# Performance work log

Hardware: AMD Instinct MI355X
Metric: run time of the kernel (lower is better)

## Reference

```python
import jax, jax.numpy as jnp
import numpy as np

NEG_FILL = -100.0  # matches torch new_full(-100.0) init for scatter-amax


def reference(x, part_labels, parts_num=16):
    # x: (n, c, s, h, w) float; part_labels: (n, s, h, w) int in [0, parts_num)
    n, c, s, h, w = x.shape
    hw = h * w
    ns = n * s
    # (n s) c (h w)
    feat = jnp.transpose(x, (0, 2, 1, 3, 4)).reshape(ns, c, hw)
    labels = part_labels.reshape(ns, hw).astype(jnp.int32)

    b3 = jnp.arange(ns)[:, None, None]          # (ns,1,1)
    ch = jnp.arange(c)[None, :, None]            # (1,c,1)
    lbl3 = labels[:, None, :]                    # (ns,1,hw) -> broadcasts to (ns,c,hw)

    pooled_sum = jnp.zeros((ns, c, parts_num), x.dtype).at[b3, ch, lbl3].add(feat)
    b2 = jnp.arange(ns)[:, None]
    pooled_count = jnp.zeros((ns, parts_num), x.dtype).at[b2, labels].add(1.0)  # (ns,P)
    pooled_max = jnp.full((ns, c, parts_num), NEG_FILL, x.dtype).at[b3, ch, lbl3].max(feat)

    count = pooled_count[:, None, :]             # (ns,1,P)
    pooled_mean = pooled_sum / jnp.maximum(count, 1.0)
    pooled_max = jnp.where(count > 0, pooled_max, 0.0)
    pooled = pooled_mean + pooled_max            # (ns,c,P)
    # (n s) c p -> n c s p
    return jnp.transpose(pooled.reshape(n, s, c, parts_num), (0, 2, 1, 3))


def setup_inputs() -> dict:
    key = jax.random.key(0)
    k1, k2 = jax.random.split(key)
    n, c, s, h, w = 16, 256, 32, 16, 11
    parts_num = 16
    x = jax.random.normal(k1, (n, c, s, h, w), dtype=jnp.float32)
    part_labels = jax.random.randint(k2, (n, s, h, w), 0, parts_num, dtype=jnp.int64)
    return {"x": x, "part_labels": part_labels, "parts_num": parts_num}
```

## Files before the change

kernel.cpp:

```cpp
#include <hip/hip_runtime.h>


constexpr int C   = 256;
constexpr int S   = 32;
constexpr int HW  = 176;
constexpr int P   = 16;
constexpr int ROW = S * HW;
constexpr int GC  = 8;
constexpr int NS2 = 2;
constexpr int PITCH = 180;
constexpr float NEG_FILL = -100.0f;

__device__ __forceinline__ void barrier_lgkm() {
    asm volatile("s_waitcnt lgkmcnt(0)\n\ts_barrier" ::: "memory");
}

__global__ __launch_bounds__(256) void hpp_kernel(
    const float* __restrict__ x,
    const int*   __restrict__ labels,
    float*       __restrict__ out)
{
    __shared__ float tile[GC * NS2 * PITCH];
    __shared__ __align__(4) unsigned char posmap[NS2][HW];
    __shared__ int cnt[NS2 * P];
    __shared__ int base[NS2 * P];

    const int tid = threadIdx.x;
    const int blk = blockIdx.x;
    const int nsp = blk >> 5, cg = blk & 31;
    const int n   = nsp >> 4, sp = nsp & 15;
    const int s   = sp * 2;

    const int* ln = labels + (size_t)(n * S + s) * HW;
    int lab0 = 0, lab1 = 0;
    if (tid < HW) { lab0 = ln[tid]; lab1 = ln[HW + tid]; }

    const float* xb = x + (size_t)(n * C + cg * GC) * ROW + s * HW;
    const int f0 = tid, f1 = tid + 256, f2 = tid + 512;
    const int r0 = f0 / 88, j0 = f0 - r0 * 88;
    const int r1 = f1 / 88, j1 = f1 - r1 * 88;
    const int r2 = f2 / 88, j2 = f2 - r2 * 88;
    float4 v0 = *(const float4*)(xb + (size_t)r0 * ROW + j0 * 4);
    float4 v1 = *(const float4*)(xb + (size_t)r1 * ROW + j1 * 4);
    float4 v2 = make_float4(0.f, 0.f, 0.f, 0.f);
    const bool has2 = (f2 < GC * 88);
    if (has2) v2 = *(const float4*)(xb + (size_t)r2 * ROW + j2 * 4);

    if (tid < NS2 * P) cnt[tid] = 0;
    barrier_lgkm();
    int a0 = 0, a1 = 0;
    if (tid < HW) {
        a0 = atomicAdd(&cnt[lab0], 1);
        a1 = atomicAdd(&cnt[P + lab1], 1);
    }
    barrier_lgkm();
    if (tid < NS2 * P) {
        int acc = 0;
        const int b0 = tid & ~(P - 1);
        for (int q = b0; q < tid; ++q) acc += cnt[q];
        base[tid] = acc;
    }
    barrier_lgkm();
    if (tid < HW) {
        posmap[0][tid] = (unsigned char)(base[lab0] + a0);
        posmap[1][tid] = (unsigned char)(base[P + lab1] + a1);
    }
    barrier_lgkm();

    {
        const int q0 = j0 * 4, s20 = (q0 >= HW), h0 = q0 - s20 * HW;
        unsigned pm0 = *(const unsigned*)&posmap[s20][h0];
        float* t0 = &tile[(r0 * 2 + s20) * PITCH];
        t0[pm0 & 0xFF] = v0.x; t0[(pm0 >> 8) & 0xFF] = v0.y;
        t0[(pm0 >> 16) & 0xFF] = v0.z; t0[pm0 >> 24] = v0.w;

        const int q1 = j1 * 4, s21 = (q1 >= HW), h1 = q1 - s21 * HW;
        unsigned pm1 = *(const unsigned*)&posmap[s21][h1];
        float* t1 = &tile[(r1 * 2 + s21) * PITCH];
        t1[pm1 & 0xFF] = v1.x; t1[(pm1 >> 8) & 0xFF] = v1.y;
        t1[(pm1 >> 16) & 0xFF] = v1.z; t1[pm1 >> 24] = v1.w;

        if (has2) {
            const int q2 = j2 * 4, s22 = (q2 >= HW), h2 = q2 - s22 * HW;
            unsigned pm2 = *(const unsigned*)&posmap[s22][h2];
            float* t2 = &tile[(r2 * 2 + s22) * PITCH];
            t2[pm2 & 0xFF] = v2.x; t2[(pm2 >> 8) & 0xFF] = v2.y;
            t2[(pm2 >> 16) & 0xFF] = v2.z; t2[pm2 >> 24] = v2.w;
        }
    }
    barrier_lgkm();

    const int p   = tid >> 4;
    const int low = tid & 15;
    const int sp2 = low & 1;
    const int c   = low >> 1;
    const int idx = sp2 * P + p;
    const int k   = cnt[idx];
    int off       = base[idx];
    const float* tc = &tile[low * PITCH];

    float s0 = 0.f, s1 = 0.f, m0 = NEG_FILL, m1 = NEG_FILL;
    int rem = k;
    int h = (4 - (off & 3)) & 3; if (h > rem) h = rem;
    if (h > 0) { float a = tc[off];     s0 += a; m0 = fmaxf(m0, a); }
    if (h > 1) { float a = tc[off + 1]; s1 += a; m1 = fmaxf(m1, a); }
    if (h > 2) { float a = tc[off + 2]; s0 += a; m0 = fmaxf(m0, a); }
    off += h; rem -= h;
    int n4 = rem >> 2;
    for (int i = 0; i < n4; ++i) {
        float4 q = *(const float4*)&tc[off];
        s0 += q.x; m0 = fmaxf(m0, q.x);
        s1 += q.y; m1 = fmaxf(m1, q.y);
        s0 += q.z; m0 = fmaxf(m0, q.z);
        s1 += q.w; m1 = fmaxf(m1, q.w);
        off += 4;
    }
    rem &= 3;
    if (rem > 0) { float a = tc[off];     s0 += a; m0 = fmaxf(m0, a); }
    if (rem > 1) { float a = tc[off + 1]; s1 += a; m1 = fmaxf(m1, a); }
    if (rem > 2) { float a = tc[off + 2]; s0 += a; m0 = fmaxf(m0, a); }

    float res = (k > 0) ? (s0 + s1) / (float)k + fmaxf(m0, m1) : 0.f;
    out[((size_t)(n * C + cg * GC + c) * S + (s + sp2)) * P + p] = res;
}

extern "C" void kernel_launch(void* const* d_in, const int* in_sizes, int n_in,
                              void* d_out, int out_size, void* d_ws, size_t ws_size,
                              hipStream_t stream) {
    const float* x      = (const float*)d_in[0];
    const int*   labels = (const int*)d_in[1];
    float*       out    = (float*)d_out;

    const int ns_total = in_sizes[1] / HW;
    const int nblk     = (ns_total / NS2) * (C / GC);
    hpp_kernel<<<nblk, 256, 0, stream>>>(x, labels, out);
}
```

Baseline: 136.3 us.

## Shrink blocks to one 64-thread wavefront, replacing barriers with LDS waitcnt fences

Each block now handles 2 channels instead of 8 using a single 64-lane wavefront, so the s_barrier instructions can be dropped and only lgkmcnt waits remain. Labels are loaded as int4 vectors and each lane histograms four labels, and the gather/reduce mapping is rebuilt for the smaller tile. This removes block-level synchronisation and raises the block count, but each block now recomputes the label histogram and posmap for 2 channels instead of 8, so that per-block work is repeated four times more often.

```diff
diff --git a/kernel.cpp b/kernel.cpp
--- a/kernel.cpp
+++ b/kernel.cpp
@@ -6,16 +6,16 @@
 constexpr int HW  = 176;
 constexpr int P   = 16;
 constexpr int ROW = S * HW;
-constexpr int GC  = 8;
+constexpr int GC  = 2;
 constexpr int NS2 = 2;
 constexpr int PITCH = 180;
 constexpr float NEG_FILL = -100.0f;
 
-__device__ __forceinline__ void barrier_lgkm() {
-    asm volatile("s_waitcnt lgkmcnt(0)\n\ts_barrier" ::: "memory");
+__device__ __forceinline__ void fence_lds() {
+    asm volatile("s_waitcnt lgkmcnt(0)" ::: "memory");
 }
 
-__global__ __launch_bounds__(256) void hpp_kernel(
+__global__ __launch_bounds__(64) void hpp_kernel(
     const float* __restrict__ x,
     const int*   __restrict__ labels,
     float*       __restrict__ out)
@@ -27,77 +27,105 @@
 
     const int tid = threadIdx.x;
     const int blk = blockIdx.x;
-    const int nsp = blk >> 5, cg = blk & 31;
+    const int cg2 = blk & 127;
+    const int nsp = blk >> 7;
     const int n   = nsp >> 4, sp = nsp & 15;
     const int s   = sp * 2;
+    const int c0  = cg2 * 2;
 
     const int* ln = labels + (size_t)(n * S + s) * HW;
-    int lab0 = 0, lab1 = 0;
-    if (tid < HW) { lab0 = ln[tid]; lab1 = ln[HW + tid]; }
+    int4 L0 = ((const int4*)ln)[tid];
+    int4 L1 = make_int4(0, 0, 0, 0);
+    const bool hasL1 = (tid < 24);
+    if (hasL1) L1 = ((const int4*)ln)[tid + 64];
 
-    const float* xb = x + (size_t)(n * C + cg * GC) * ROW + s * HW;
-    const int f0 = tid, f1 = tid + 256, f2 = tid + 512;
-    const int r0 = f0 / 88, j0 = f0 - r0 * 88;
-    const int r1 = f1 / 88, j1 = f1 - r1 * 88;
-    const int r2 = f2 / 88, j2 = f2 - r2 * 88;
-    float4 v0 = *(const float4*)(xb + (size_t)r0 * ROW + j0 * 4);
+    const float* xb = x + (size_t)(n * C + c0) * ROW + s * HW;
+    const int j0 = tid;
+    const int r1 = (tid < 24) ? 0 : 1;
+    const int j1 = (tid < 24) ? tid + 64 : tid - 24;
+    const int j2 = tid + 40;
+    const bool has2 = (tid < 48);
+    float4 v0 = *(const float4*)(xb + (size_t)0 * ROW + j0 * 4);
     float4 v1 = *(const float4*)(xb + (size_t)r1 * ROW + j1 * 4);
     float4 v2 = make_float4(0.f, 0.f, 0.f, 0.f);
-    const bool has2 = (f2 < GC * 88);
-    if (has2) v2 = *(const float4*)(xb + (size_t)r2 * ROW + j2 * 4);
+    if (has2) v2 = *(const float4*)(xb + (size_t)1 * ROW + j2 * 4);
 
     if (tid < NS2 * P) cnt[tid] = 0;
-    barrier_lgkm();
-    int a0 = 0, a1 = 0;
-    if (tid < HW) {
-        a0 = atomicAdd(&cnt[lab0], 1);
-        a1 = atomicAdd(&cnt[P + lab1], 1);
+    fence_lds();
+    const int row0 = (tid >= 44);
+    int a0, a1, a2, a3;
+    {
+        int* c = &cnt[row0 * P];
+        a0 = atomicAdd(&c[L0.x], 1);
+        a1 = atomicAdd(&c[L0.y], 1);
+        a2 = atomicAdd(&c[L0.z], 1);
+        a3 = atomicAdd(&c[L0.w], 1);
     }
-    barrier_lgkm();
+    int b0 = 0, b1 = 0, b2 = 0, b3 = 0;
+    if (hasL1) {
+        int* c = &cnt[P];
+        b0 = atomicAdd(&c[L1.x], 1);
+        b1 = atomicAdd(&c[L1.y], 1);
+        b2 = atomicAdd(&c[L1.z], 1);
+        b3 = atomicAdd(&c[L1.w], 1);
+    }
+    fence_lds();
     if (tid < NS2 * P) {
         int acc = 0;
-        const int b0 = tid & ~(P - 1);
-        for (int q = b0; q < tid; ++q) acc += cnt[q];
+        const int g0 = tid & ~(P - 1);
+        for (int q = g0; q < tid; ++q) acc += cnt[q];
         base[tid] = acc;
     }
-    barrier_lgkm();
-    if (tid < HW) {
-        posmap[0][tid] = (unsigned char)(base[lab0] + a0);
-        posmap[1][tid] = (unsigned char)(base[P + lab1] + a1);
+    fence_lds();
+    {
+        const int hw0 = (tid * 4) - row0 * 176;
+        const int* bs = &base[row0 * P];
+        posmap[row0][hw0    ] = (unsigned char)(bs[L0.x] + a0);
+        posmap[row0][hw0 + 1] = (unsigned char)(bs[L0.y] + a1);
+        posmap[row0][hw0 + 2] = (unsigned char)(bs[L0.z] + a2);
+        posmap[row0][hw0 + 3] = (unsigned char)(bs[L0.w] + a3);
+        if (hasL1) {
+            const int hw1 = 80 + tid * 4;
+            const int* b1s = &base[P];
+            posmap[1][hw1    ] = (unsigned char)(b1s[L1.x] + b0);
+            posmap[1][hw1 + 1] = (unsigned char)(b1s[L1.y] + b1);
+            posmap[1][hw1 + 2] = (unsigned char)(b1s[L1.z] + b2);
+            posmap[1][hw1 + 3] = (unsigned char)(b1s[L1.w] + b3);
+        }
     }
-    barrier_lgkm();
+    fence_lds();
 
     {
-        const int q0 = j0 * 4, s20 = (q0 >= HW), h0 = q0 - s20 * HW;
+        const int s20 = (j0 >= 44), h0 = j0 * 4 - s20 * 176;
         unsigned pm0 = *(const unsigned*)&posmap[s20][h0];
-        float* t0 = &tile[(r0 * 2 + s20) * PITCH];
+        float* t0 = &tile[(0 * 2 + s20) * PITCH];
         t0[pm0 & 0xFF] = v0.x; t0[(pm0 >> 8) & 0xFF] = v0.y;
         t0[(pm0 >> 16) & 0xFF] = v0.z; t0[pm0 >> 24] = v0.w;
 
-        const int q1 = j1 * 4, s21 = (q1 >= HW), h1 = q1 - s21 * HW;
+        const int s21 = (j1 >= 44), h1 = j1 * 4 - s21 * 176;
         unsigned pm1 = *(const unsigned*)&posmap[s21][h1];
         float* t1 = &tile[(r1 * 2 + s21) * PITCH];
         t1[pm1 & 0xFF] = v1.x; t1[(pm1 >> 8) & 0xFF] = v1.y;
         t1[(pm1 >> 16) & 0xFF] = v1.z; t1[pm1 >> 24] = v1.w;
 
         if (has2) {
-            const int q2 = j2 * 4, s22 = (q2 >= HW), h2 = q2 - s22 * HW;
+            const int s22 = (j2 >= 44), h2 = j2 * 4 - s22 * 176;
             unsigned pm2 = *(const unsigned*)&posmap[s22][h2];
-            float* t2 = &tile[(r2 * 2 + s22) * PITCH];
+            float* t2 = &tile[(1 * 2 + s22) * PITCH];
             t2[pm2 & 0xFF] = v2.x; t2[(pm2 >> 8) & 0xFF] = v2.y;
             t2[(pm2 >> 16) & 0xFF] = v2.z; t2[pm2 >> 24] = v2.w;
         }
     }
-    barrier_lgkm();
+    fence_lds();
 
-    const int p   = tid >> 4;
-    const int low = tid & 15;
-    const int sp2 = low & 1;
-    const int c   = low >> 1;
+    const int p   = tid >> 2;
+    const int lo  = tid & 3;
+    const int cp  = lo >> 1;
+    const int sp2 = lo & 1;
     const int idx = sp2 * P + p;
     const int k   = cnt[idx];
     int off       = base[idx];
-    const float* tc = &tile[low * PITCH];
+    const float* tc = &tile[(cp * 2 + sp2) * PITCH];
 
     float s0 = 0.f, s1 = 0.f, m0 = NEG_FILL, m1 = NEG_FILL;
     int rem = k;
@@ -121,7 +149,7 @@
     if (rem > 2) { float a = tc[off + 2]; s0 += a; m0 = fmaxf(m0, a); }
 
     float res = (k > 0) ? (s0 + s1) / (float)k + fmaxf(m0, m1) : 0.f;
-    out[((size_t)(n * C + cg * GC + c) * S + (s + sp2)) * P + p] = res;
+    out[((size_t)(n * C + c0 + cp) * S + (s + sp2)) * P + p] = res;
 }
 
 extern "C" void kernel_launch(void* const* d_in, const int* in_sizes, int n_in,
@@ -133,5 +161,5 @@
 
     const int ns_total = in_sizes[1] / HW;
     const int nblk     = (ns_total / NS2) * (C / GC);
-    hpp_kernel<<<nblk, 256, 0, stream>>>(x, labels, out);
+    hpp_kernel<<<nblk, 64, 0, stream>>>(x, labels, out);
 }
```

Result: no change. 136.8 us (+0.3%).
